# Optimization experiments

Hardware: AMD Instinct MI355X
Metric: run time of the kernel (lower is better)

Reference implementation:

```python
import jax, jax.numpy as jnp
import numpy as np

T, D, H, E, TOP_K = 8192, 1024, 4096, 8, 2


def setup_inputs() -> dict:
    key = jax.random.key(0)
    ks = jax.random.split(key, 4)
    s_in = 1.0 / np.sqrt(D)
    s_hid = 1.0 / np.sqrt(H)
    return {
        "x": jax.random.normal(ks[0], (T, D), dtype=jnp.float32),
        "Wg": jax.random.normal(ks[1], (D, E), dtype=jnp.float32) * s_in,
        "W1": jax.random.normal(ks[2], (E, D, H), dtype=jnp.float32) * s_in,
        "b1": jnp.zeros((E, H), dtype=jnp.float32),
        "W2": jax.random.normal(ks[3], (E, H, D), dtype=jnp.float32) * s_hid,
        "b2": jnp.zeros((E, D), dtype=jnp.float32),
    }


def _moe_forward(x, Wg, W1, b1, W2, b2):
    # Gating: router logits -> top-k -> renormalized softmax over selected experts
    logits = x @ Wg                                   # [T, E]
    top_vals, top_idx = jax.lax.top_k(logits, TOP_K)  # [T, K]
    gates = jax.nn.softmax(top_vals, axis=-1)         # [T, K]
    # Dense [T, E] combine weights (zero for unselected experts)
    w = jnp.zeros_like(logits).at[jnp.arange(x.shape[0])[:, None], top_idx].set(gates)
    # Per-expert 2-layer MLP computed densely, combined by gate weights
    h = jax.nn.relu(jnp.einsum("td,edh->teh", x, W1) + b1[None])   # [T, E, H]
    y = jnp.einsum("teh,ehd->ted", h, W2) + b2[None]               # [T, E, D]
    return jnp.einsum("te,ted->td", w, y)                          # [T, D]


def reference(x, Wg, W1, b1, W2, b2):
    # Deterministic main path of OuroborosMoELayer.forward: the topology-gated
    # domain shift fires only on a rare scalar condition; standard path is the
    # top-k MoE dispatch/combine.
    return _moe_forward(x, Wg, W1, b1, W2, b2)
```

## Files before the change

### kernel.cpp

```cpp
#include <hip/hip_runtime.h>
#include <hip/hip_bf16.h>

#define TT 8192
#define DD 1024
#define HH 4096
#define EE 8

typedef unsigned short u16;
typedef unsigned int u32;
typedef float fx4 __attribute__((ext_vector_type(4)));
typedef short s8v __attribute__((ext_vector_type(8)));
typedef int i4v __attribute__((ext_vector_type(4)));
typedef u16 u16x4 __attribute__((ext_vector_type(4)));

__device__ __forceinline__ u16 f2bf(float x) {
  union { float f; u32 u; } c; c.f = x;
  u32 r = (c.u + 0x7FFFu + ((c.u >> 16) & 1u)) >> 16;
  return (u16)r;
}

__device__ __forceinline__ void gl2lds16(const void* g, void* l) {
  __builtin_amdgcn_global_load_lds(
      (const __attribute__((address_space(1))) void*)g,
      (__attribute__((address_space(3))) void*)l, 16, 0, 0);
}

__global__ void zero_meta(int* counts) {
  if (threadIdx.x < EE) counts[threadIdx.x] = 0;
}

__global__ void convert_x_kernel(const float* __restrict__ x, u16* __restrict__ xb) {
  int i = (blockIdx.x * 256 + threadIdx.x) * 4;
  float4 v = *(const float4*)(x + i);
  u16x4 o;
  o[0] = f2bf(v.x); o[1] = f2bf(v.y); o[2] = f2bf(v.z); o[3] = f2bf(v.w);
  *(u16x4*)(xb + i) = o;
}

template<int R, int C>
__global__ void transpose_convert(const float* __restrict__ W, u16* __restrict__ Wt) {
  __shared__ float tile[64][65];
  const int e = blockIdx.z;
  const float* We = W + (size_t)e * R * C;
  u16* Wte = Wt + (size_t)e * R * C;
  const int r0 = blockIdx.y * 64, c0 = blockIdx.x * 64;
  const int tid = threadIdx.x;
  const int a = tid >> 4, b4 = (tid & 15) * 4;
#pragma unroll
  for (int i = 0; i < 4; ++i) {
    int rr = a + i * 16;
    float4 v = *(const float4*)(We + (size_t)(r0 + rr) * C + c0 + b4);
    tile[rr][b4 + 0] = v.x; tile[rr][b4 + 1] = v.y;
    tile[rr][b4 + 2] = v.z; tile[rr][b4 + 3] = v.w;
  }
  __syncthreads();
#pragma unroll
  for (int i = 0; i < 4; ++i) {
    int cc = a + i * 16;
    u16x4 o;
    o[0] = f2bf(tile[b4 + 0][cc]);
    o[1] = f2bf(tile[b4 + 1][cc]);
    o[2] = f2bf(tile[b4 + 2][cc]);
    o[3] = f2bf(tile[b4 + 3][cc]);
    *(u16x4*)(Wte + (size_t)(c0 + cc) * R + r0 + b4) = o;
  }
}

__global__ void router_kernel(const float* __restrict__ x, const float* __restrict__ Wg,
                              int* __restrict__ topIdx, float* __restrict__ gates,
                              int* __restrict__ counts) {
  __shared__ float wg[EE][DD + 1];
  const int tid = threadIdx.x;
  for (int i = tid; i < DD * EE; i += 256) wg[i & 7][i >> 3] = Wg[i];
  __syncthreads();
  const int w = tid >> 6, lane = tid & 63;
  const int t = blockIdx.x * 4 + w;
  double acc[EE];
#pragma unroll
  for (int e = 0; e < EE; ++e) acc[e] = 0.0;
  const float* xr = x + (size_t)t * DD;
  for (int i = 0; i < DD / 64; ++i) {
    int d = i * 64 + lane;
    double xv = (double)xr[d];
#pragma unroll
    for (int e = 0; e < EE; ++e) acc[e] += xv * (double)wg[e][d];
  }
#pragma unroll
  for (int e = 0; e < EE; ++e) {
    double v = acc[e];
#pragma unroll
    for (int s = 32; s > 0; s >>= 1) v += __shfl_xor(v, s, 64);
    acc[e] = v;
  }
  if (lane == 0) {
    float v0 = -3.4e38f, v1 = -3.4e38f; int i0 = 0, i1 = 0;
#pragma unroll
    for (int e = 0; e < EE; ++e) {
      float v = (float)acc[e];
      if (v > v0) { v1 = v0; i1 = i0; v0 = v; i0 = e; }
      else if (v > v1) { v1 = v; i1 = e; }
    }
    float ee = expf(v1 - v0);
    float g0 = 1.f / (1.f + ee);
    float g1 = ee / (1.f + ee);
    topIdx[t * 2 + 0] = i0; topIdx[t * 2 + 1] = i1;
    gates[t * 2 + 0] = g0; gates[t * 2 + 1] = g1;
    atomicAdd(&counts[i0], 1);
    atomicAdd(&counts[i1], 1);
  }
}

__global__ void prefix_kernel(const int* __restrict__ counts, int* __restrict__ offsets) {
  if (threadIdx.x == 0) {
    int s = 0;
    for (int e = 0; e < EE; ++e) { offsets[e] = s; s += counts[e]; }
    offsets[EE] = s;
  }
}

__global__ void scatter_det(const int* __restrict__ topIdx, const float* __restrict__ gates,
                            const int* __restrict__ offsets, int* __restrict__ entryTok,
                            float* __restrict__ entryGate) {
  const int e = blockIdx.x;
  const int tid = threadIdx.x;
  const int lane = tid & 63, w = tid >> 6;
  __shared__ int base;
  __shared__ int wsum[16];
  __shared__ int woff[16];
  __shared__ int chunktot;
  if (tid == 0) base = offsets[e];
  __syncthreads();
  for (int t0 = 0; t0 < TT; t0 += 1024) {
    int t = t0 + tid;
    int k = -1;
    if (topIdx[t * 2 + 0] == e) k = 0;
    else if (topIdx[t * 2 + 1] == e) k = 1;
    unsigned long long m = __ballot(k >= 0);
    int pre = __popcll(m & ((1ULL << lane) - 1ULL));
    if (lane == 0) wsum[w] = __popcll(m);
    __syncthreads();
    if (tid == 0) {
      int s = 0;
      for (int i = 0; i < 16; ++i) { woff[i] = s; s += wsum[i]; }
      chunktot = s;
    }
    __syncthreads();
    if (k >= 0) {
      int p = base + woff[w] + pre;
      entryTok[p] = t;
      entryGate[p] = gates[t * 2 + k];
    }
    __syncthreads();
    if (tid == 0) base += chunktot;
    __syncthreads();
  }
}

template<int EPI, int K, int N>
__global__ __launch_bounds__(256) void moe_gemm_fast(
    const u16* __restrict__ A, const u16* __restrict__ Bt,
    const float* __restrict__ bias,
    const int* __restrict__ counts, const int* __restrict__ offsets,
    const int* __restrict__ entryTok, const float* __restrict__ entryGate,
    u16* __restrict__ hout, float* __restrict__ out) {
  const int e = blockIdx.z;
  const int cnt = counts[e];
  const int mbase = blockIdx.y * 128;
  if (mbase >= cnt) return;
  const int off = offsets[e];
  const int nbase = blockIdx.x * 128;
  const int tid = threadIdx.x;
  const int w = tid >> 6, lane = tid & 63;

  __shared__ __align__(16) u16 Asm[128][64];
  __shared__ __align__(16) u16 Bsm[128][64];
  __shared__ int rowTok[128];
  __shared__ float rowGate[128];

  if (tid < 128) {
    int m = mbase + tid;
    int valid = (m < cnt) ? 1 : 0;
    rowTok[tid] = valid ? entryTok[off + m] : 0;
    rowGate[tid] = valid ? entryGate[off + m] : 0.f;
  }

  const u16* asrc[4];
  const u16* bsrc[4];
  u16* adst[4];
  u16* bdst[4];
#pragma unroll
  for (int j = 0; j < 4; ++j) {
    int c = j * 256 + tid;
    int row = c >> 3;
    int col = ((c & 7) ^ (row & 7)) * 8;
    int gm = mbase + row;
    int mm = (gm < cnt) ? gm : (cnt - 1);
    const u16* ab;
    if (EPI == 0) ab = A + (size_t)entryTok[off + mm] * K;
    else          ab = A + (size_t)(off + mm) * K;
    asrc[j] = ab + col;
    bsrc[j] = Bt + (size_t)e * N * K + (size_t)(nbase + row) * K + col;
    int chunkbase = j * 256 + w * 64;
    adst[j] = &Asm[0][0] + (size_t)chunkbase * 8;
    bdst[j] = &Bsm[0][0] + (size_t)chunkbase * 8;
  }

  const int wm = (w >> 1) * 64, wn = (w & 1) * 64;
  const int fl = lane & 15, fh = lane >> 4;
  const int fswz = fl & 7;

  fx4 acc[4][4];
#pragma unroll
  for (int mi = 0; mi < 4; ++mi)
#pragma unroll
    for (int ni = 0; ni < 4; ++ni)
      acc[mi][ni] = (fx4){0.f, 0.f, 0.f, 0.f};

  for (int kt = 0; kt < K; kt += 64) {
#pragma unroll
    for (int j = 0; j < 4; ++j) {
      gl2lds16(asrc[j] + kt, adst[j]);
      gl2lds16(bsrc[j] + kt, bdst[j]);
    }
    __syncthreads();
#pragma unroll
    for (int ks = 0; ks < 2; ++ks) {
      s8v af[4], bf[4];
#pragma unroll
      for (int i = 0; i < 4; ++i)
        af[i] = *(const s8v*)&Asm[wm + i * 16 + fl][((ks * 4 + fh) ^ fswz) * 8];
#pragma unroll
      for (int i = 0; i < 4; ++i)
        bf[i] = *(const s8v*)&Bsm[wn + i * 16 + fl][((ks * 4 + fh) ^ fswz) * 8];
#pragma unroll
      for (int mi = 0; mi < 4; ++mi)
#pragma unroll
        for (int ni = 0; ni < 4; ++ni)
          acc[mi][ni] = __builtin_amdgcn_mfma_f32_16x16x32_bf16(af[mi], bf[ni], acc[mi][ni], 0, 0, 0);
    }
    __syncthreads();
  }

#pragma unroll
  for (int mi = 0; mi < 4; ++mi) {
#pragma unroll
    for (int ni = 0; ni < 4; ++ni) {
      int n = nbase + wn + ni * 16 + fl;
      float bv = bias[e * N + n];
#pragma unroll
      for (int b = 0; b < 4; ++b) {
        int tm = wm + mi * 16 + fh * 4 + b;
        int gm = mbase + tm;
        if (gm < cnt) {
          float v = acc[mi][ni][b] + bv;
          if (EPI == 0) {
            v = v > 0.f ? v : 0.f;
            hout[(size_t)(off + gm) * N + n] = f2bf(v);
          } else {
            atomicAdd(&out[(size_t)rowTok[tm] * N + n], v * rowGate[tm]);
          }
        }
      }
    }
  }
}

template<int EPI, int K, int N>
__global__ __launch_bounds__(256) void moe_gemm_slow(
    const u16* __restrict__ A, const float* __restrict__ Bw,
    const float* __restrict__ bias,
    const int* __restrict__ counts, const int* __restrict__ offsets,
    const int* __restrict__ entryTok, const float* __restrict__ entryGate,
    u16* __restrict__ hout, float* __restrict__ out) {
  const int e = blockIdx.z;
  const int cnt = counts[e];
  const int mbase = blockIdx.y * 128;
  if (mbase >= cnt) return;
  const int off = offsets[e];
  const int nbase = blockIdx.x * 128;
  const int tid = threadIdx.x;

  __shared__ u16 Asm[128][72];
  __shared__ u16 Bsm[128][72];
  __shared__ int rowTok[128];
  __shared__ float rowGate[128];

  if (tid < 128) {
    int m = mbase + tid;
    int valid = (m < cnt) ? 1 : 0;
    rowTok[tid] = valid ? entryTok[off + m] : -1;
    rowGate[tid] = valid ? entryGate[off + m] : 0.f;
  }
  __syncthreads();

  const int r = tid >> 1, half = tid & 1;
  const u16* arow;
  if (EPI == 0) {
    int tk = rowTok[r];
    arow = (tk >= 0) ? (A + (size_t)tk * K) : (const u16*)0;
  } else {
    int m = mbase + r;
    arow = (m < cnt) ? (A + (size_t)(off + m) * K) : (const u16*)0;
  }
  const int bk = tid >> 2;
  const int bn0 = (tid & 3) * 32;
  const float* bsrc = Bw + (size_t)e * K * N + (size_t)bk * N + nbase + bn0;

  const int w = tid >> 6, lane = tid & 63;
  const int wm = (w >> 1) * 64, wn = (w & 1) * 64;
  const int fl = lane & 15, fh = lane >> 4;

  fx4 acc[4][4];
#pragma unroll
  for (int mi = 0; mi < 4; ++mi)
#pragma unroll
    for (int ni = 0; ni < 4; ++ni)
      acc[mi][ni] = (fx4){0.f, 0.f, 0.f, 0.f};

  for (int kt = 0; kt < K; kt += 64) {
#pragma unroll
    for (int j = 0; j < 4; ++j) {
      int col = half * 32 + j * 8;
      i4v va = arow ? *(const i4v*)(arow + kt + col) : (i4v){0, 0, 0, 0};
      *(i4v*)&Asm[r][col] = va;
    }
#pragma unroll
    for (int j = 0; j < 8; ++j) {
      float4 v = *(const float4*)(bsrc + (size_t)kt * N + j * 4);
      Bsm[bn0 + j * 4 + 0][bk] = f2bf(v.x);
      Bsm[bn0 + j * 4 + 1][bk] = f2bf(v.y);
      Bsm[bn0 + j * 4 + 2][bk] = f2bf(v.z);
      Bsm[bn0 + j * 4 + 3][bk] = f2bf(v.w);
    }
    __syncthreads();
#pragma unroll
    for (int ks = 0; ks < 2; ++ks) {
      s8v af[4], bf[4];
#pragma unroll
      for (int i = 0; i < 4; ++i)
        af[i] = *(const s8v*)&Asm[wm + i * 16 + fl][ks * 32 + fh * 8];
#pragma unroll
      for (int i = 0; i < 4; ++i)
        bf[i] = *(const s8v*)&Bsm[wn + i * 16 + fl][ks * 32 + fh * 8];
#pragma unroll
      for (int mi = 0; mi < 4; ++mi)
#pragma unroll
        for (int ni = 0; ni < 4; ++ni)
          acc[mi][ni] = __builtin_amdgcn_mfma_f32_16x16x32_bf16(af[mi], bf[ni], acc[mi][ni], 0, 0, 0);
    }
    __syncthreads();
  }

#pragma unroll
  for (int mi = 0; mi < 4; ++mi) {
#pragma unroll
    for (int ni = 0; ni < 4; ++ni) {
      int n = nbase + wn + ni * 16 + fl;
      float bv = bias[e * N + n];
#pragma unroll
      for (int b = 0; b < 4; ++b) {
        int tm = wm + mi * 16 + fh * 4 + b;
        int gm = mbase + tm;
        if (gm < cnt) {
          float v = acc[mi][ni][b] + bv;
          if (EPI == 0) {
            v = v > 0.f ? v : 0.f;
            hout[(size_t)(off + gm) * N + n] = f2bf(v);
          } else {
            atomicAdd(&out[(size_t)rowTok[tm] * N + n], v * rowGate[tm]);
          }
        }
      }
    }
  }
}

extern "C" void kernel_launch(void* const* d_in, const int* in_sizes, int n_in,
                              void* d_out, int out_size, void* d_ws, size_t ws_size,
                              hipStream_t stream) {
  const float* x  = (const float*)d_in[0];
  const float* Wg = (const float*)d_in[1];
  const float* W1 = (const float*)d_in[2];
  const float* b1 = (const float*)d_in[3];
  const float* W2 = (const float*)d_in[4];
  const float* b2 = (const float*)d_in[5];
  float* out = (float*)d_out;

  char* ws = (char*)d_ws;
  int* counts  = (int*)(ws + 0);
  int* offsets = (int*)(ws + 128);
  size_t o = 256;
  int* topIdx = (int*)(ws + o);        o += (size_t)2 * TT * 4;
  float* gates = (float*)(ws + o);     o += (size_t)2 * TT * 4;
  int* entryTok = (int*)(ws + o);      o += (size_t)2 * TT * 4;
  float* entryGate = (float*)(ws + o); o += (size_t)2 * TT * 4;
  u16* xb  = (u16*)(ws + o);           o += (size_t)TT * DD * 2;

  const size_t FAST_REQ = (size_t)218366208;
  const bool fast = (ws_size >= FAST_REQ);

  hipMemsetAsync(d_out, 0, (size_t)TT * DD * 4, stream);
  zero_meta<<<1, 64, 0, stream>>>(counts);
  convert_x_kernel<<<(TT * DD / 4) / 256, 256, 0, stream>>>(x, xb);
  router_kernel<<<TT / 4, 256, 0, stream>>>(x, Wg, topIdx, gates, counts);
  prefix_kernel<<<1, 1, 0, stream>>>(counts, offsets);
  scatter_det<<<EE, 1024, 0, stream>>>(topIdx, gates, offsets, entryTok, entryGate);

  if (fast) {
    u16* wbuf = (u16*)(ws + o);
    u16* hbuf = (u16*)(ws + o + (size_t)EE * DD * HH * 2);
    transpose_convert<DD, HH><<<dim3(HH / 64, DD / 64, EE), 256, 0, stream>>>(W1, wbuf);
    moe_gemm_fast<0, DD, HH><<<dim3(HH / 128, TT / 128, EE), 256, 0, stream>>>(
        xb, wbuf, b1, counts, offsets, entryTok, entryGate, hbuf, nullptr);
    transpose_convert<HH, DD><<<dim3(DD / 64, HH / 64, EE), 256, 0, stream>>>(W2, wbuf);
    moe_gemm_fast<1, HH, DD><<<dim3(DD / 128, TT / 128, EE), 256, 0, stream>>>(
        hbuf, wbuf, b2, counts, offsets, entryTok, entryGate, nullptr, out);
  } else {
    u16* hbuf = (u16*)(ws + o);
    moe_gemm_slow<0, DD, HH><<<dim3(HH / 128, TT / 128, EE), 256, 0, stream>>>(
        xb, W1, b1, counts, offsets, entryTok, entryGate, hbuf, nullptr);
    moe_gemm_slow<1, HH, DD><<<dim3(DD / 128, TT / 128, EE), 256, 0, stream>>>(
        hbuf, W2, b2, counts, offsets, entryTok, entryGate, nullptr, out);
  }
}
```

Baseline: 850.1 us.

## Enlarge MoE GEMM tiles to 256x256 with double-buffered LDS prefetch

The expert GEMM kernel now uses 512-thread blocks computing 256x256 output tiles, with each wave holding an 8x4 grid of MFMA accumulators. It also double-buffers the A and B LDS tiles so the next k-slice is loaded while the current one is multiplied. The goal is more operand reuse per byte loaded and hiding global-to-LDS latency. In exchange, LDS use grows to about 128KB per block, which limits occupancy to one block per CU, and there are fewer blocks per expert. The down-projection epilogue also reads token and gate values from global memory instead of a shared-memory cache.

```diff
diff --git a/kernel.cpp b/kernel.cpp
--- a/kernel.cpp
+++ b/kernel.cpp
@@ -157,7 +157,7 @@
 }
 
 template<int EPI, int K, int N>
-__global__ __launch_bounds__(256) void moe_gemm_fast(
+__global__ __launch_bounds__(512, 2) void moe_gemm_fast(
     const u16* __restrict__ A, const u16* __restrict__ Bt,
     const float* __restrict__ bias,
     const int* __restrict__ counts, const int* __restrict__ offsets,
@@ -165,75 +165,79 @@
     u16* __restrict__ hout, float* __restrict__ out) {
   const int e = blockIdx.z;
   const int cnt = counts[e];
-  const int mbase = blockIdx.y * 128;
+  const int mbase = blockIdx.y * 256;
   if (mbase >= cnt) return;
   const int off = offsets[e];
-  const int nbase = blockIdx.x * 128;
+  const int nbase = blockIdx.x * 256;
   const int tid = threadIdx.x;
   const int w = tid >> 6, lane = tid & 63;
 
-  __shared__ __align__(16) u16 Asm[128][64];
-  __shared__ __align__(16) u16 Bsm[128][64];
-  __shared__ int rowTok[128];
-  __shared__ float rowGate[128];
-
-  if (tid < 128) {
-    int m = mbase + tid;
-    int valid = (m < cnt) ? 1 : 0;
-    rowTok[tid] = valid ? entryTok[off + m] : 0;
-    rowGate[tid] = valid ? entryGate[off + m] : 0.f;
-  }
-
-  const u16* asrc[4];
-  const u16* bsrc[4];
-  u16* adst[4];
-  u16* bdst[4];
-#pragma unroll
-  for (int j = 0; j < 4; ++j) {
-    int c = j * 256 + tid;
+  __shared__ __align__(16) u16 Asm[2][256][64];
+  __shared__ __align__(16) u16 Bsm[2][256][64];
+
+  const u16* src[8];
+  u32 dstoff[8];
+#pragma unroll
+  for (int j = 0; j < 8; ++j) {
+    int c = (j & 3) * 512 + tid;
     int row = c >> 3;
     int col = ((c & 7) ^ (row & 7)) * 8;
-    int gm = mbase + row;
-    int mm = (gm < cnt) ? gm : (cnt - 1);
-    const u16* ab;
-    if (EPI == 0) ab = A + (size_t)entryTok[off + mm] * K;
-    else          ab = A + (size_t)(off + mm) * K;
-    asrc[j] = ab + col;
-    bsrc[j] = Bt + (size_t)e * N * K + (size_t)(nbase + row) * K + col;
-    int chunkbase = j * 256 + w * 64;
-    adst[j] = &Asm[0][0] + (size_t)chunkbase * 8;
-    bdst[j] = &Bsm[0][0] + (size_t)chunkbase * 8;
-  }
-
-  const int wm = (w >> 1) * 64, wn = (w & 1) * 64;
+    if (j < 4) {
+      int gm = mbase + row;
+      int mm = (gm < cnt) ? gm : (cnt - 1);
+      const u16* ab = (EPI == 0) ? (A + (size_t)entryTok[off + mm] * K)
+                                 : (A + (size_t)(off + mm) * K);
+      src[j] = ab + col;
+    } else {
+      src[j] = Bt + (size_t)e * N * K + (size_t)(nbase + row) * K + col;
+    }
+    dstoff[j] = (u32)c * 16;
+  }
+
+  const int wr = w >> 2, wc = w & 3;
+  const int rm = wr * 128, cn = wc * 64;
   const int fl = lane & 15, fh = lane >> 4;
   const int fswz = fl & 7;
 
-  fx4 acc[4][4];
-#pragma unroll
-  for (int mi = 0; mi < 4; ++mi)
+  fx4 acc[8][4];
+#pragma unroll
+  for (int mi = 0; mi < 8; ++mi)
 #pragma unroll
     for (int ni = 0; ni < 4; ++ni)
       acc[mi][ni] = (fx4){0.f, 0.f, 0.f, 0.f};
 
-  for (int kt = 0; kt < K; kt += 64) {
-#pragma unroll
-    for (int j = 0; j < 4; ++j) {
-      gl2lds16(asrc[j] + kt, adst[j]);
-      gl2lds16(bsrc[j] + kt, bdst[j]);
-    }
-    __syncthreads();
+#pragma unroll
+  for (int j = 0; j < 4; ++j)
+    gl2lds16(src[j], (char*)&Asm[0][0][0] + dstoff[j]);
+#pragma unroll
+  for (int j = 4; j < 8; ++j)
+    gl2lds16(src[j], (char*)&Bsm[0][0][0] + dstoff[j]);
+  __syncthreads();
+
+  const int NST = K / 64;
+  for (int step = 0; step < NST; ++step) {
+    const int cur = step & 1;
+    if (step + 1 < NST) {
+      const int kt = (step + 1) * 64;
+#pragma unroll
+      for (int j = 0; j < 4; ++j)
+        gl2lds16(src[j] + kt, (char*)&Asm[cur ^ 1][0][0] + dstoff[j]);
+#pragma unroll
+      for (int j = 4; j < 8; ++j)
+        gl2lds16(src[j] + kt, (char*)&Bsm[cur ^ 1][0][0] + dstoff[j]);
+    }
 #pragma unroll
     for (int ks = 0; ks < 2; ++ks) {
-      s8v af[4], bf[4];
+      const int slot = ((ks * 4 + fh) ^ fswz) * 8;
+      s8v af[8], bf[4];
+#pragma unroll
+      for (int i = 0; i < 8; ++i)
+        af[i] = *(const s8v*)&Asm[cur][rm + i * 16 + fl][slot];
 #pragma unroll
       for (int i = 0; i < 4; ++i)
-        af[i] = *(const s8v*)&Asm[wm + i * 16 + fl][((ks * 4 + fh) ^ fswz) * 8];
-#pragma unroll
-      for (int i = 0; i < 4; ++i)
-        bf[i] = *(const s8v*)&Bsm[wn + i * 16 + fl][((ks * 4 + fh) ^ fswz) * 8];
-#pragma unroll
-      for (int mi = 0; mi < 4; ++mi)
+        bf[i] = *(const s8v*)&Bsm[cur][cn + i * 16 + fl][slot];
+#pragma unroll
+      for (int mi = 0; mi < 8; ++mi)
 #pragma unroll
         for (int ni = 0; ni < 4; ++ni)
           acc[mi][ni] = __builtin_amdgcn_mfma_f32_16x16x32_bf16(af[mi], bf[ni], acc[mi][ni], 0, 0, 0);
@@ -242,14 +246,14 @@
   }
 
 #pragma unroll
-  for (int mi = 0; mi < 4; ++mi) {
+  for (int mi = 0; mi < 8; ++mi) {
 #pragma unroll
     for (int ni = 0; ni < 4; ++ni) {
-      int n = nbase + wn + ni * 16 + fl;
+      int n = nbase + cn + ni * 16 + fl;
       float bv = bias[e * N + n];
 #pragma unroll
       for (int b = 0; b < 4; ++b) {
-        int tm = wm + mi * 16 + fh * 4 + b;
+        int tm = rm + mi * 16 + fh * 4 + b;
         int gm = mbase + tm;
         if (gm < cnt) {
           float v = acc[mi][ni][b] + bv;
@@ -257,7 +261,7 @@
             v = v > 0.f ? v : 0.f;
             hout[(size_t)(off + gm) * N + n] = f2bf(v);
           } else {
-            atomicAdd(&out[(size_t)rowTok[tm] * N + n], v * rowGate[tm]);
+            atomicAdd(&out[(size_t)entryTok[off + gm] * N + n], v * entryGate[off + gm]);
           }
         }
       }
@@ -410,10 +414,10 @@
     u16* wbuf = (u16*)(ws + o);
     u16* hbuf = (u16*)(ws + o + (size_t)EE * DD * HH * 2);
     transpose_convert<DD, HH><<<dim3(HH / 64, DD / 64, EE), 256, 0, stream>>>(W1, wbuf);
-    moe_gemm_fast<0, DD, HH><<<dim3(HH / 128, TT / 128, EE), 256, 0, stream>>>(
+    moe_gemm_fast<0, DD, HH><<<dim3(HH / 256, TT / 256, EE), 512, 0, stream>>>(
         xb, wbuf, b1, counts, offsets, entryTok, entryGate, hbuf, nullptr);
     transpose_convert<HH, DD><<<dim3(DD / 64, HH / 64, EE), 256, 0, stream>>>(W2, wbuf);
-    moe_gemm_fast<1, HH, DD><<<dim3(DD / 128, TT / 128, EE), 256, 0, stream>>>(
+    moe_gemm_fast<1, HH, DD><<<dim3(DD / 256, TT / 256, EE), 512, 0, stream>>>(
         hbuf, wbuf, b2, counts, offsets, entryTok, entryGate, nullptr, out);
   } else {
     u16* hbuf = (u16*)(ws + o);
```

Measured after the change: 925.3 us. 8.8% more time.

## Double-buffer LDS tiles, batch M tiles per block, and swizzle block order

Applied to the files above, without the earlier changes.

Turns the MoE grouped GEMM into a double-buffered pipeline that uses explicit vmcnt waits and raw barriers, so global-to-LDS loads for the next K-step overlap the MFMA work. In the first GEMM each block now walks several M tiles (MT=4) over a 1D grid, reusing the B tile columns and reducing block launch overhead. Block indices are remapped across XCDs to improve L2 locality. This adds LDS use (two buffers) and more complex control flow, and it relies on hand-tuned wait counts.

```diff
diff --git a/kernel.cpp b/kernel.cpp
--- a/kernel.cpp
+++ b/kernel.cpp
@@ -156,53 +156,73 @@
   }
 }
 
-template<int EPI, int K, int N>
+template<int EPI, int K, int N, int MT>
 __global__ __launch_bounds__(256) void moe_gemm_fast(
     const u16* __restrict__ A, const u16* __restrict__ Bt,
     const float* __restrict__ bias,
     const int* __restrict__ counts, const int* __restrict__ offsets,
     const int* __restrict__ entryTok, const float* __restrict__ entryGate,
     u16* __restrict__ hout, float* __restrict__ out) {
-  const int e = blockIdx.z;
+  constexpr int KS = K / 64;
+  constexpr int NX = N / 128;
+  constexpr int NYG = 64 / MT;
+  constexpr int nwg = NX * NYG * EE;
+
+  const int p = blockIdx.x;
+  const int l = (p & 7) * (nwg >> 3) + (p >> 3);
+  const int yg = l % NYG;
+  const int t1 = l / NYG;
+  const int xb = t1 % NX;
+  const int e  = t1 / NX;
+
   const int cnt = counts[e];
-  const int mbase = blockIdx.y * 128;
-  if (mbase >= cnt) return;
+  const int mb0 = yg * (MT * 128);
+  if (mb0 >= cnt) return;
   const int off = offsets[e];
-  const int nbase = blockIdx.x * 128;
+  const int nbase = xb * 128;
   const int tid = threadIdx.x;
   const int w = tid >> 6, lane = tid & 63;
-
-  __shared__ __align__(16) u16 Asm[128][64];
-  __shared__ __align__(16) u16 Bsm[128][64];
-  __shared__ int rowTok[128];
-  __shared__ float rowGate[128];
-
-  if (tid < 128) {
-    int m = mbase + tid;
-    int valid = (m < cnt) ? 1 : 0;
-    rowTok[tid] = valid ? entryTok[off + m] : 0;
-    rowGate[tid] = valid ? entryGate[off + m] : 0.f;
-  }
-
-  const u16* asrc[4];
+  const int tmax = (cnt - mb0 + 127) >> 7;
+  const int G = (tmax < MT ? tmax : MT) * KS;
+
+  __shared__ __align__(16) u16 Asm[2][128][64];
+  __shared__ __align__(16) u16 Bsm[2][128][64];
+
   const u16* bsrc[4];
-  u16* adst[4];
-  u16* bdst[4];
+  const u16* cur_a[4];
+  u32 dstoff[4];
 #pragma unroll
   for (int j = 0; j < 4; ++j) {
     int c = j * 256 + tid;
     int row = c >> 3;
     int col = ((c & 7) ^ (row & 7)) * 8;
-    int gm = mbase + row;
-    int mm = (gm < cnt) ? gm : (cnt - 1);
-    const u16* ab;
-    if (EPI == 0) ab = A + (size_t)entryTok[off + mm] * K;
-    else          ab = A + (size_t)(off + mm) * K;
-    asrc[j] = ab + col;
     bsrc[j] = Bt + (size_t)e * N * K + (size_t)(nbase + row) * K + col;
-    int chunkbase = j * 256 + w * 64;
-    adst[j] = &Asm[0][0] + (size_t)chunkbase * 8;
-    bdst[j] = &Bsm[0][0] + (size_t)chunkbase * 8;
+    dstoff[j] = (u32)c * 16;
+  }
+
+#define ADVA(TAU)                                                          \
+  {                                                                        \
+    _Pragma("unroll") for (int j = 0; j < 4; ++j) {                        \
+      int c_ = j * 256 + tid;                                              \
+      int row_ = c_ >> 3;                                                  \
+      int col_ = ((c_ & 7) ^ (row_ & 7)) * 8;                              \
+      int gm_ = mb0 + (TAU) * 128 + row_;                                  \
+      int mm_ = (gm_ < cnt) ? gm_ : (cnt - 1);                             \
+      int tok_ = (EPI == 0) ? entryTok[off + mm_] : (off + mm_);           \
+      cur_a[j] = A + (size_t)tok_ * K + col_;                              \
+    }                                                                      \
+  }
+
+#define STAGE(GG)                                                          \
+  {                                                                        \
+    const int s_ = (GG) & 1;                                               \
+    const int kofs_ = ((GG) & (KS - 1)) * 64;                              \
+    char* ab_ = (char*)&Asm[s_][0][0];                                     \
+    char* bb_ = (char*)&Bsm[s_][0][0];                                     \
+    _Pragma("unroll") for (int j = 0; j < 4; ++j)                          \
+        gl2lds16(cur_a[j] + kofs_, ab_ + dstoff[j]);                       \
+    _Pragma("unroll") for (int j = 0; j < 4; ++j)                          \
+        gl2lds16(bsrc[j] + kofs_, bb_ + dstoff[j]);                        \
   }
 
   const int wm = (w >> 1) * 64, wn = (w & 1) * 64;
@@ -216,53 +236,84 @@
     for (int ni = 0; ni < 4; ++ni)
       acc[mi][ni] = (fx4){0.f, 0.f, 0.f, 0.f};
 
-  for (int kt = 0; kt < K; kt += 64) {
-#pragma unroll
-    for (int j = 0; j < 4; ++j) {
-      gl2lds16(asrc[j] + kt, adst[j]);
-      gl2lds16(bsrc[j] + kt, bdst[j]);
-    }
-    __syncthreads();
+  ADVA(0);
+  STAGE(0);
+  STAGE(1);
+
+  for (int g = 0; g < G; ++g) {
+    if (g + 1 < G) {
+      asm volatile("s_waitcnt vmcnt(8)" ::: "memory");
+    } else {
+      asm volatile("s_waitcnt vmcnt(0)" ::: "memory");
+    }
+    __builtin_amdgcn_s_barrier();
+    const int cur = g & 1;
+    __builtin_amdgcn_s_setprio(1);
 #pragma unroll
     for (int ks = 0; ks < 2; ++ks) {
+      const int slot = ((ks * 4 + fh) ^ fswz) * 8;
       s8v af[4], bf[4];
 #pragma unroll
       for (int i = 0; i < 4; ++i)
-        af[i] = *(const s8v*)&Asm[wm + i * 16 + fl][((ks * 4 + fh) ^ fswz) * 8];
+        af[i] = *(const s8v*)&Asm[cur][wm + i * 16 + fl][slot];
 #pragma unroll
       for (int i = 0; i < 4; ++i)
-        bf[i] = *(const s8v*)&Bsm[wn + i * 16 + fl][((ks * 4 + fh) ^ fswz) * 8];
+        bf[i] = *(const s8v*)&Bsm[cur][wn + i * 16 + fl][slot];
 #pragma unroll
       for (int mi = 0; mi < 4; ++mi)
 #pragma unroll
         for (int ni = 0; ni < 4; ++ni)
           acc[mi][ni] = __builtin_amdgcn_mfma_f32_16x16x32_bf16(af[mi], bf[ni], acc[mi][ni], 0, 0, 0);
     }
-    __syncthreads();
-  }
-
-#pragma unroll
-  for (int mi = 0; mi < 4; ++mi) {
-#pragma unroll
-    for (int ni = 0; ni < 4; ++ni) {
-      int n = nbase + wn + ni * 16 + fl;
-      float bv = bias[e * N + n];
-#pragma unroll
-      for (int b = 0; b < 4; ++b) {
-        int tm = wm + mi * 16 + fh * 4 + b;
-        int gm = mbase + tm;
-        if (gm < cnt) {
-          float v = acc[mi][ni][b] + bv;
-          if (EPI == 0) {
-            v = v > 0.f ? v : 0.f;
-            hout[(size_t)(off + gm) * N + n] = f2bf(v);
-          } else {
-            atomicAdd(&out[(size_t)rowTok[tm] * N + n], v * rowGate[tm]);
+    __builtin_amdgcn_s_setprio(0);
+    __builtin_amdgcn_s_barrier();
+    asm volatile("" ::: "memory");
+    const int gn = g + 2;
+    if (gn < G) {
+      if ((gn & (KS - 1)) == 0) ADVA(gn / KS);
+      STAGE(gn);
+    }
+    if ((g & (KS - 1)) == KS - 1) {
+      const int mbase = mb0 + (g / KS) * 128;
+#pragma unroll
+      for (int mi = 0; mi < 4; ++mi) {
+#pragma unroll
+        for (int b = 0; b < 4; ++b) {
+          int tm = wm + mi * 16 + fh * 4 + b;
+          int gm = mbase + tm;
+          if (gm < cnt) {
+            if (EPI == 0) {
+              u16* hrow = hout + (size_t)(off + gm) * N;
+#pragma unroll
+              for (int ni = 0; ni < 4; ++ni) {
+                int n = nbase + wn + ni * 16 + fl;
+                float v = acc[mi][ni][b] + bias[e * N + n];
+                v = v > 0.f ? v : 0.f;
+                hrow[n] = f2bf(v);
+              }
+            } else {
+              int tok = entryTok[off + gm];
+              float gate = entryGate[off + gm];
+              float* orow = out + (size_t)tok * N;
+#pragma unroll
+              for (int ni = 0; ni < 4; ++ni) {
+                int n = nbase + wn + ni * 16 + fl;
+                float v = (acc[mi][ni][b] + bias[e * N + n]) * gate;
+                atomicAdd(&orow[n], v);
+              }
+            }
           }
         }
       }
-    }
-  }
+#pragma unroll
+      for (int mi = 0; mi < 4; ++mi)
+#pragma unroll
+        for (int ni = 0; ni < 4; ++ni)
+          acc[mi][ni] = (fx4){0.f, 0.f, 0.f, 0.f};
+    }
+  }
+#undef STAGE
+#undef ADVA
 }
 
 template<int EPI, int K, int N>
@@ -410,10 +461,10 @@
     u16* wbuf = (u16*)(ws + o);
     u16* hbuf = (u16*)(ws + o + (size_t)EE * DD * HH * 2);
     transpose_convert<DD, HH><<<dim3(HH / 64, DD / 64, EE), 256, 0, stream>>>(W1, wbuf);
-    moe_gemm_fast<0, DD, HH><<<dim3(HH / 128, TT / 128, EE), 256, 0, stream>>>(
+    moe_gemm_fast<0, DD, HH, 4><<<(HH / 128) * 16 * EE, 256, 0, stream>>>(
         xb, wbuf, b1, counts, offsets, entryTok, entryGate, hbuf, nullptr);
     transpose_convert<HH, DD><<<dim3(DD / 64, HH / 64, EE), 256, 0, stream>>>(W2, wbuf);
-    moe_gemm_fast<1, HH, DD><<<dim3(DD / 128, TT / 128, EE), 256, 0, stream>>>(
+    moe_gemm_fast<1, HH, DD, 1><<<(DD / 128) * 64 * EE, 256, 0, stream>>>(
         hbuf, wbuf, b2, counts, offsets, entryTok, entryGate, nullptr, out);
   } else {
     u16* hbuf = (u16*)(ws + o);
```

Result: slower. 899.3 us (+5.8%).

## Fuse x conversion into router, specialize MoE GEMMs with multi-tile and split-K

Applied to the files above, without the earlier changes.

The bf16 conversion of x moves into the router kernel, which removes a separate launch and a second read of x. The first expert GEMM now has each block loop over two M tiles, which halves the grid and amortizes the B-pointer setup. It also adds occupancy launch bounds. The second GEMM uses 512-thread blocks with a 128x256 tile and a 2-way split-K across the grid z-dimension, and accumulates through atomics with the bias added only by the first K half. This doubles the atomic traffic on the output and changes register pressure and tile shapes.

```diff
diff --git a/kernel.cpp b/kernel.cpp
--- a/kernel.cpp
+++ b/kernel.cpp
@@ -27,14 +27,6 @@
 
 __global__ void zero_meta(int* counts) {
   if (threadIdx.x < EE) counts[threadIdx.x] = 0;
-}
-
-__global__ void convert_x_kernel(const float* __restrict__ x, u16* __restrict__ xb) {
-  int i = (blockIdx.x * 256 + threadIdx.x) * 4;
-  float4 v = *(const float4*)(x + i);
-  u16x4 o;
-  o[0] = f2bf(v.x); o[1] = f2bf(v.y); o[2] = f2bf(v.z); o[3] = f2bf(v.w);
-  *(u16x4*)(xb + i) = o;
 }
 
 template<int R, int C>
@@ -68,7 +60,7 @@
 
 __global__ void router_kernel(const float* __restrict__ x, const float* __restrict__ Wg,
                               int* __restrict__ topIdx, float* __restrict__ gates,
-                              int* __restrict__ counts) {
+                              int* __restrict__ counts, u16* __restrict__ xb) {
   __shared__ float wg[EE][DD + 1];
   const int tid = threadIdx.x;
   for (int i = tid; i < DD * EE; i += 256) wg[i & 7][i >> 3] = Wg[i];
@@ -79,9 +71,12 @@
 #pragma unroll
   for (int e = 0; e < EE; ++e) acc[e] = 0.0;
   const float* xr = x + (size_t)t * DD;
+  u16* xbr = xb + (size_t)t * DD;
   for (int i = 0; i < DD / 64; ++i) {
     int d = i * 64 + lane;
-    double xv = (double)xr[d];
+    float xf = xr[d];
+    xbr[d] = f2bf(xf);
+    double xv = (double)xf;
 #pragma unroll
     for (int e = 0; e < EE; ++e) acc[e] += xv * (double)wg[e][d];
   }
@@ -156,56 +151,154 @@
   }
 }
 
-template<int EPI, int K, int N>
-__global__ __launch_bounds__(256) void moe_gemm_fast(
+template<int K, int N, int MT>
+__global__ __launch_bounds__(256, 5) void moe_gemm1(
+    const u16* __restrict__ A, const u16* __restrict__ Bt,
+    const float* __restrict__ bias,
+    const int* __restrict__ counts, const int* __restrict__ offsets,
+    const int* __restrict__ entryTok, u16* __restrict__ hout) {
+  const int e = blockIdx.z;
+  const int cnt = counts[e];
+  const int mb0 = blockIdx.y * (128 * MT);
+  if (mb0 >= cnt) return;
+  const int off = offsets[e];
+  const int nbase = blockIdx.x * 128;
+  const int tid = threadIdx.x;
+  const int w = tid >> 6, lane = tid & 63;
+
+  __shared__ __align__(16) u16 Asm[128][64];
+  __shared__ __align__(16) u16 Bsm[128][64];
+
+  const u16* bsrc[4];
+  u32 dstoff[4];
+#pragma unroll
+  for (int j = 0; j < 4; ++j) {
+    int c = j * 256 + tid;
+    int row = c >> 3;
+    int col = ((c & 7) ^ (row & 7)) * 8;
+    bsrc[j] = Bt + (size_t)e * N * K + (size_t)(nbase + row) * K + col;
+    dstoff[j] = (u32)c * 16;
+  }
+
+  const int wm = (w >> 1) * 64, wn = (w & 1) * 64;
+  const int fl = lane & 15, fh = lane >> 4;
+  const int fswz = fl & 7;
+
+  const int rem = (cnt - mb0 + 127) >> 7;
+  const int ntau = rem < MT ? rem : MT;
+
+  for (int tau = 0; tau < ntau; ++tau) {
+    const int mbase = mb0 + tau * 128;
+    const u16* asrc[4];
+#pragma unroll
+    for (int j = 0; j < 4; ++j) {
+      int c = j * 256 + tid;
+      int row = c >> 3;
+      int col = ((c & 7) ^ (row & 7)) * 8;
+      int gm = mbase + row;
+      int mm = (gm < cnt) ? gm : (cnt - 1);
+      asrc[j] = A + (size_t)entryTok[off + mm] * K + col;
+    }
+
+    fx4 acc[4][4];
+#pragma unroll
+    for (int mi = 0; mi < 4; ++mi)
+#pragma unroll
+      for (int ni = 0; ni < 4; ++ni)
+        acc[mi][ni] = (fx4){0.f, 0.f, 0.f, 0.f};
+
+    for (int kt = 0; kt < K; kt += 64) {
+#pragma unroll
+      for (int j = 0; j < 4; ++j) {
+        gl2lds16(asrc[j] + kt, (char*)&Asm[0][0] + dstoff[j]);
+        gl2lds16(bsrc[j] + kt, (char*)&Bsm[0][0] + dstoff[j]);
+      }
+      __syncthreads();
+#pragma unroll
+      for (int ks = 0; ks < 2; ++ks) {
+        const int slot = ((ks * 4 + fh) ^ fswz) * 8;
+        s8v af[4], bf[4];
+#pragma unroll
+        for (int i = 0; i < 4; ++i)
+          af[i] = *(const s8v*)&Asm[wm + i * 16 + fl][slot];
+#pragma unroll
+        for (int i = 0; i < 4; ++i)
+          bf[i] = *(const s8v*)&Bsm[wn + i * 16 + fl][slot];
+#pragma unroll
+        for (int mi = 0; mi < 4; ++mi)
+#pragma unroll
+          for (int ni = 0; ni < 4; ++ni)
+            acc[mi][ni] = __builtin_amdgcn_mfma_f32_16x16x32_bf16(af[mi], bf[ni], acc[mi][ni], 0, 0, 0);
+      }
+      __syncthreads();
+    }
+
+#pragma unroll
+    for (int mi = 0; mi < 4; ++mi) {
+#pragma unroll
+      for (int b = 0; b < 4; ++b) {
+        int tm = wm + mi * 16 + fh * 4 + b;
+        int gm = mbase + tm;
+        if (gm < cnt) {
+          u16* hrow = hout + (size_t)(off + gm) * N;
+#pragma unroll
+          for (int ni = 0; ni < 4; ++ni) {
+            int n = nbase + wn + ni * 16 + fl;
+            float v = acc[mi][ni][b] + bias[e * N + n];
+            v = v > 0.f ? v : 0.f;
+            hrow[n] = f2bf(v);
+          }
+        }
+      }
+    }
+    __syncthreads();
+  }
+}
+
+template<int K, int N, int KSPLIT>
+__global__ __launch_bounds__(512, 6) void moe_gemm2(
     const u16* __restrict__ A, const u16* __restrict__ Bt,
     const float* __restrict__ bias,
     const int* __restrict__ counts, const int* __restrict__ offsets,
     const int* __restrict__ entryTok, const float* __restrict__ entryGate,
-    u16* __restrict__ hout, float* __restrict__ out) {
-  const int e = blockIdx.z;
+    float* __restrict__ out) {
+  const int zc = blockIdx.z;
+  const int e = zc & 7, kh = zc >> 3;
   const int cnt = counts[e];
   const int mbase = blockIdx.y * 128;
   if (mbase >= cnt) return;
   const int off = offsets[e];
-  const int nbase = blockIdx.x * 128;
+  const int nbase = blockIdx.x * 256;
+  const int k0 = kh * (K / KSPLIT);
   const int tid = threadIdx.x;
   const int w = tid >> 6, lane = tid & 63;
 
   __shared__ __align__(16) u16 Asm[128][64];
-  __shared__ __align__(16) u16 Bsm[128][64];
-  __shared__ int rowTok[128];
-  __shared__ float rowGate[128];
-
-  if (tid < 128) {
-    int m = mbase + tid;
-    int valid = (m < cnt) ? 1 : 0;
-    rowTok[tid] = valid ? entryTok[off + m] : 0;
-    rowGate[tid] = valid ? entryGate[off + m] : 0.f;
-  }
-
-  const u16* asrc[4];
+  __shared__ __align__(16) u16 Bsm[256][64];
+
+  const u16* asrc[2];
   const u16* bsrc[4];
-  u16* adst[4];
-  u16* bdst[4];
-#pragma unroll
-  for (int j = 0; j < 4; ++j) {
-    int c = j * 256 + tid;
+  u32 adst[2], bdst[4];
+#pragma unroll
+  for (int j = 0; j < 2; ++j) {
+    int c = j * 512 + tid;
     int row = c >> 3;
     int col = ((c & 7) ^ (row & 7)) * 8;
     int gm = mbase + row;
     int mm = (gm < cnt) ? gm : (cnt - 1);
-    const u16* ab;
-    if (EPI == 0) ab = A + (size_t)entryTok[off + mm] * K;
-    else          ab = A + (size_t)(off + mm) * K;
-    asrc[j] = ab + col;
-    bsrc[j] = Bt + (size_t)e * N * K + (size_t)(nbase + row) * K + col;
-    int chunkbase = j * 256 + w * 64;
-    adst[j] = &Asm[0][0] + (size_t)chunkbase * 8;
-    bdst[j] = &Bsm[0][0] + (size_t)chunkbase * 8;
-  }
-
-  const int wm = (w >> 1) * 64, wn = (w & 1) * 64;
+    asrc[j] = A + (size_t)(off + mm) * K + k0 + col;
+    adst[j] = (u32)c * 16;
+  }
+#pragma unroll
+  for (int j = 0; j < 4; ++j) {
+    int c = j * 512 + tid;
+    int row = c >> 3;
+    int col = ((c & 7) ^ (row & 7)) * 8;
+    bsrc[j] = Bt + (size_t)e * N * K + (size_t)(nbase + row) * K + k0 + col;
+    bdst[j] = (u32)c * 16;
+  }
+
+  const int wm = (w >> 2) * 64, wn = (w & 3) * 64;
   const int fl = lane & 15, fh = lane >> 4;
   const int fswz = fl & 7;
 
@@ -216,22 +309,24 @@
     for (int ni = 0; ni < 4; ++ni)
       acc[mi][ni] = (fx4){0.f, 0.f, 0.f, 0.f};
 
-  for (int kt = 0; kt < K; kt += 64) {
-#pragma unroll
-    for (int j = 0; j < 4; ++j) {
-      gl2lds16(asrc[j] + kt, adst[j]);
-      gl2lds16(bsrc[j] + kt, bdst[j]);
-    }
+  for (int kt = 0; kt < K / KSPLIT; kt += 64) {
+#pragma unroll
+    for (int j = 0; j < 2; ++j)
+      gl2lds16(asrc[j] + kt, (char*)&Asm[0][0] + adst[j]);
+#pragma unroll
+    for (int j = 0; j < 4; ++j)
+      gl2lds16(bsrc[j] + kt, (char*)&Bsm[0][0] + bdst[j]);
     __syncthreads();
 #pragma unroll
     for (int ks = 0; ks < 2; ++ks) {
+      const int slot = ((ks * 4 + fh) ^ fswz) * 8;
       s8v af[4], bf[4];
 #pragma unroll
       for (int i = 0; i < 4; ++i)
-        af[i] = *(const s8v*)&Asm[wm + i * 16 + fl][((ks * 4 + fh) ^ fswz) * 8];
+        af[i] = *(const s8v*)&Asm[wm + i * 16 + fl][slot];
 #pragma unroll
       for (int i = 0; i < 4; ++i)
-        bf[i] = *(const s8v*)&Bsm[wn + i * 16 + fl][((ks * 4 + fh) ^ fswz) * 8];
+        bf[i] = *(const s8v*)&Bsm[wn + i * 16 + fl][slot];
 #pragma unroll
       for (int mi = 0; mi < 4; ++mi)
 #pragma unroll
@@ -244,21 +339,18 @@
 #pragma unroll
   for (int mi = 0; mi < 4; ++mi) {
 #pragma unroll
-    for (int ni = 0; ni < 4; ++ni) {
-      int n = nbase + wn + ni * 16 + fl;
-      float bv = bias[e * N + n];
-#pragma unroll
-      for (int b = 0; b < 4; ++b) {
-        int tm = wm + mi * 16 + fh * 4 + b;
-        int gm = mbase + tm;
-        if (gm < cnt) {
-          float v = acc[mi][ni][b] + bv;
-          if (EPI == 0) {
-            v = v > 0.f ? v : 0.f;
-            hout[(size_t)(off + gm) * N + n] = f2bf(v);
-          } else {
-            atomicAdd(&out[(size_t)rowTok[tm] * N + n], v * rowGate[tm]);
-          }
+    for (int b = 0; b < 4; ++b) {
+      int tm = wm + mi * 16 + fh * 4 + b;
+      int gm = mbase + tm;
+      if (gm < cnt) {
+        int tok = entryTok[off + gm];
+        float gate = entryGate[off + gm];
+        float* orow = out + (size_t)tok * N;
+#pragma unroll
+        for (int ni = 0; ni < 4; ++ni) {
+          int n = nbase + wn + ni * 16 + fl;
+          float v = acc[mi][ni][b] + (kh == 0 ? bias[e * N + n] : 0.f);
+          atomicAdd(&orow[n], v * gate);
         }
       }
     }
@@ -375,6 +467,14 @@
   }
 }
 
+__global__ void convert_x_kernel(const float* __restrict__ x, u16* __restrict__ xb) {
+  int i = (blockIdx.x * 256 + threadIdx.x) * 4;
+  float4 v = *(const float4*)(x + i);
+  u16x4 o;
+  o[0] = f2bf(v.x); o[1] = f2bf(v.y); o[2] = f2bf(v.z); o[3] = f2bf(v.w);
+  *(u16x4*)(xb + i) = o;
+}
+
 extern "C" void kernel_launch(void* const* d_in, const int* in_sizes, int n_in,
                               void* d_out, int out_size, void* d_ws, size_t ws_size,
                               hipStream_t stream) {
@@ -401,8 +501,7 @@
 
   hipMemsetAsync(d_out, 0, (size_t)TT * DD * 4, stream);
   zero_meta<<<1, 64, 0, stream>>>(counts);
-  convert_x_kernel<<<(TT * DD / 4) / 256, 256, 0, stream>>>(x, xb);
-  router_kernel<<<TT / 4, 256, 0, stream>>>(x, Wg, topIdx, gates, counts);
+  router_kernel<<<TT / 4, 256, 0, stream>>>(x, Wg, topIdx, gates, counts, xb);
   prefix_kernel<<<1, 1, 0, stream>>>(counts, offsets);
   scatter_det<<<EE, 1024, 0, stream>>>(topIdx, gates, offsets, entryTok, entryGate);
 
@@ -410,11 +509,11 @@
     u16* wbuf = (u16*)(ws + o);
     u16* hbuf = (u16*)(ws + o + (size_t)EE * DD * HH * 2);
     transpose_convert<DD, HH><<<dim3(HH / 64, DD / 64, EE), 256, 0, stream>>>(W1, wbuf);
-    moe_gemm_fast<0, DD, HH><<<dim3(HH / 128, TT / 128, EE), 256, 0, stream>>>(
-        xb, wbuf, b1, counts, offsets, entryTok, entryGate, hbuf, nullptr);
+    moe_gemm1<DD, HH, 2><<<dim3(HH / 128, TT / 256, EE), 256, 0, stream>>>(
+        xb, wbuf, b1, counts, offsets, entryTok, hbuf);
     transpose_convert<HH, DD><<<dim3(DD / 64, HH / 64, EE), 256, 0, stream>>>(W2, wbuf);
-    moe_gemm_fast<1, HH, DD><<<dim3(DD / 128, TT / 128, EE), 256, 0, stream>>>(
-        hbuf, wbuf, b2, counts, offsets, entryTok, entryGate, nullptr, out);
+    moe_gemm2<HH, DD, 2><<<dim3(DD / 256, TT / 128, EE * 2), 512, 0, stream>>>(
+        hbuf, wbuf, b2, counts, offsets, entryTok, entryGate, out);
   } else {
     u16* hbuf = (u16*)(ws + o);
     moe_gemm_slow<0, DD, HH><<<dim3(HH / 128, TT / 128, EE), 256, 0, stream>>>(
```

Measured after the change: 2.592 ms. +204.8%, slower.
